# Performance work log

Measured on AMD Instinct MI355X. Metric: run time of the kernel, lower is better.

## Reference

```python
import jax, jax.numpy as jnp
import numpy as np
import math

B, H, S, DIM = 1, 16, 2048, 128

def _clin(xr, xi, wr, wi, br, bi):
    # complex linear: F.linear semantics -> x @ W.T
    out_r = xr @ wr.T - xi @ wi.T + br
    out_i = xr @ wi.T + xi @ wr.T + bi
    return out_r, out_i

def setup_inputs() -> dict:
    key = jax.random.key(0)
    ks = jax.random.split(key, 32)
    shp = (B, H, S, DIM)
    names = ["q_r", "q_i", "k_r", "k_i", "v_r", "v_i", "pe_q_r", "pe_q_i", "pe_k_r", "pe_k_i"]
    d = {n: jax.random.normal(ks[i], shp, jnp.float32) for i, n in enumerate(names)}
    wscale = 1.0 / math.sqrt(DIM)
    i = 10
    for p in ["q", "k", "v", "g", "o"]:
        d[p + "w_r"] = jax.random.normal(ks[i], (DIM, DIM), jnp.float32) * wscale; i += 1
        d[p + "w_i"] = jax.random.normal(ks[i], (DIM, DIM), jnp.float32) * wscale; i += 1
        d[p + "b_r"] = jnp.zeros((DIM,), jnp.float32)
        d[p + "b_i"] = jnp.zeros((DIM,), jnp.float32)
    return d

def reference(q_r, q_i, k_r, k_i, v_r, v_i, pe_q_r, pe_q_i, pe_k_r, pe_k_i,
              qw_r, qw_i, qb_r, qb_i, kw_r, kw_i, kb_r, kb_i,
              vw_r, vw_i, vb_r, vb_i, gw_r, gw_i, gb_r, gb_i,
              ow_r, ow_i, ob_r, ob_i):
    scale = DIM ** -0.5
    qr, qi = _clin(q_r, q_i, qw_r, qw_i, qb_r, qb_i)
    kr, ki = _clin(k_r, k_i, kw_r, kw_i, kb_r, kb_i)
    vr, vi = _clin(v_r, v_i, vw_r, vw_i, vb_r, vb_i)
    qr = qr + pe_q_r; qi = qi + pe_q_i
    kr = kr + pe_k_r; ki = ki + pe_k_i
    # complex QK^H -> real/imag parts, shapes [B,H,S,S]
    sr = jnp.einsum('bhqd,bhkd->bhqk', qr, kr) + jnp.einsum('bhqd,bhkd->bhqk', qi, ki)
    si = jnp.einsum('bhqd,bhkd->bhqk', qi, kr) - jnp.einsum('bhqd,bhkd->bhqk', qr, ki)
    scores = jnp.sqrt(sr * sr + si * si + 1e-8) * scale  # magnitude scores
    attn = jax.nn.softmax(scores, axis=-1)
    ar = attn @ vr
    ai = attn @ vi
    gr, gi = _clin(q_r, q_i, gw_r, gw_i, gb_r, gb_i)  # gate from raw q
    gar = gr * ar - gi * ai
    gai = gr * ai + gi * ar
    out_r, out_i = _clin(gar, gai, ow_r, ow_i, ob_r, ob_i)
    return (out_r, out_i, gr, gi)
```

## Files before the change

kernel.cpp:

```cpp
#include <hip/hip_runtime.h>
#include <math.h>

#define HH 16
#define SS 2048
#define DD 128
#define NROWS (HH * SS)
#define OUTSZ (HH * SS * DD)

typedef __attribute__((ext_vector_type(8))) short bf16x8;
typedef __attribute__((ext_vector_type(4))) float f32x4;
typedef __attribute__((ext_vector_type(8))) unsigned short u16x8;

#define MFMA16(a, b, c) __builtin_amdgcn_mfma_f32_16x16x32_bf16(a, b, c, 0, 0, 0)

__device__ __forceinline__ unsigned short f2bf(float f) {
    unsigned u = __float_as_uint(f);
    return (unsigned short)((u + 0x7FFFu + ((u >> 16) & 1u)) >> 16);
}
__device__ __forceinline__ bf16x8 negf(bf16x8 a) {
    bf16x8 r;
#pragma unroll
    for (int j = 0; j < 8; ++j) r[j] = (short)(a[j] ^ (short)0x8000);
    return r;
}

struct ClinPtrs {
    const float* xr; const float* xi;
    const float* wr; const float* wi;
    const float* br; const float* bi;
    const float* per; const float* pei;
    void* yr; void* yi;
    int outbf;
};

struct RawA { float4 v[16]; };

__device__ __forceinline__ void load_tile(RawA& r, const float* xr, const float* xi,
                                          long rbase, int quad) {
#pragma unroll
    for (int dk = 0; dk < 4; ++dk) {
        const long o = rbase + dk * 32 + quad * 8;
        r.v[dk * 4 + 0] = *(const float4*)(xr + o);
        r.v[dk * 4 + 1] = *(const float4*)(xr + o + 4);
        r.v[dk * 4 + 2] = *(const float4*)(xi + o);
        r.v[dk * 4 + 3] = *(const float4*)(xi + o + 4);
    }
}
__device__ __forceinline__ void conv_tile(const RawA& r, bf16x8* xrf, bf16x8* xif) {
#pragma unroll
    for (int dk = 0; dk < 4; ++dk) {
        const float4 a0 = r.v[dk * 4 + 0], a1 = r.v[dk * 4 + 1];
        const float4 b0 = r.v[dk * 4 + 2], b1 = r.v[dk * 4 + 3];
        const float fr[8] = {a0.x, a0.y, a0.z, a0.w, a1.x, a1.y, a1.z, a1.w};
        const float fi[8] = {b0.x, b0.y, b0.z, b0.w, b1.x, b1.y, b1.z, b1.w};
#pragma unroll
        for (int j = 0; j < 8; ++j) {
            xrf[dk][j] = (short)f2bf(fr[j]);
            xif[dk][j] = (short)f2bf(fi[j]);
        }
    }
}

__global__ __launch_bounds__(512, 2)
void clin_stream(ClinPtrs P0, ClinPtrs P1, ClinPtrs P2, ClinPtrs P3) {
    __shared__ unsigned short wsh[2][DD][136];

    const int py = blockIdx.y;
    const ClinPtrs P = (py == 0) ? P0 : (py == 1) ? P1 : (py == 2) ? P2 : P3;

    const int t = threadIdx.x;
    const int w = t >> 6, lane = t & 63;
    const int lm = lane & 15, quad = lane >> 4;
    const long blockRow0 = (long)blockIdx.x * 512;

    RawA rawA, rawB;
    load_tile(rawA, P.xr, P.xi, (blockRow0 + w * 16 + lm) * DD, quad);

#pragma unroll
    for (int u = 0; u < 8; ++u) {
        const int f = t + 512 * u;
        const int c = f >> 11;
        const int rem = f & 2047;
        const int row = rem >> 4;
        const int g8 = (rem & 15) * 8;
        const float* src = (c ? P.wi : P.wr) + (long)row * DD + g8;
        const float4 a = *(const float4*)src;
        const float4 b = *(const float4*)(src + 4);
        unsigned short tmp[8] = {f2bf(a.x), f2bf(a.y), f2bf(a.z), f2bf(a.w),
                                 f2bf(b.x), f2bf(b.y), f2bf(b.z), f2bf(b.w)};
        *(u16x8*)&wsh[c][row][g8] = *(u16x8*)tmp;
    }
    __syncthreads();

    const f32x4 z = {0.f, 0.f, 0.f, 0.f};

#pragma unroll
    for (int tt = 0; tt < 4; ++tt) {
        RawA& cur = (tt & 1) ? rawB : rawA;
        RawA& nxt = (tt & 1) ? rawA : rawB;
        if (tt < 3)
            load_tile(nxt, P.xr, P.xi,
                      (blockRow0 + (tt + 1) * 128 + w * 16 + lm) * DD, quad);

        bf16x8 xrf[4], xif[4];
        conv_tile(cur, xrf, xif);

        f32x4 Or[8], Oi[8];
#pragma unroll
        for (int nt = 0; nt < 8; ++nt) { Or[nt] = z; Oi[nt] = z; }

#pragma unroll
        for (int dk = 0; dk < 4; ++dk) {
            const bf16x8 nxi = negf(xif[dk]);
            const int off = dk * 32 + quad * 8;
#pragma unroll
            for (int nt = 0; nt < 8; ++nt) {
                const bf16x8 wrf = *(bf16x8*)&wsh[0][nt * 16 + lm][off];
                const bf16x8 wif = *(bf16x8*)&wsh[1][nt * 16 + lm][off];
                Or[nt] = MFMA16(xrf[dk], wrf, Or[nt]);
                Or[nt] = MFMA16(nxi,     wif, Or[nt]);
                Oi[nt] = MFMA16(xrf[dk], wif, Oi[nt]);
                Oi[nt] = MFMA16(xif[dk], wrf, Oi[nt]);
            }
        }

        const long m0 = blockRow0 + tt * 128 + w * 16;
#pragma unroll
        for (int nt = 0; nt < 8; ++nt) {
            const int c = nt * 16 + lm;
            const float bra = P.br[c], bia = P.bi[c];
#pragma unroll
            for (int reg = 0; reg < 4; ++reg) {
                const long R = m0 + quad * 4 + reg;
                float vr = Or[nt][reg] + bra;
                float vi = Oi[nt][reg] + bia;
                if (P.per != nullptr) {
                    vr += P.per[R * DD + c];
                    vi += P.pei[R * DD + c];
                }
                if (P.outbf) {
                    ((unsigned short*)P.yr)[R * DD + c] = f2bf(vr);
                    ((unsigned short*)P.yi)[R * DD + c] = f2bf(vi);
                } else {
                    ((float*)P.yr)[R * DD + c] = vr;
                    ((float*)P.yi)[R * DD + c] = vi;
                }
            }
        }
    }
}

__global__ __launch_bounds__(512, 2)
void clin_gate(const float* __restrict__ xr, const float* __restrict__ xi,
               const float* __restrict__ gr, const float* __restrict__ gi,
               const float* __restrict__ wr, const float* __restrict__ wi,
               const float* __restrict__ br, const float* __restrict__ bi,
               float* __restrict__ yr, float* __restrict__ yi) {
    __shared__ unsigned short wsh[2][DD][136];

    const int t = threadIdx.x;
#pragma unroll
    for (int u = 0; u < 8; ++u) {
        const int f = t + 512 * u;
        const int c = f >> 11;
        const int rem = f & 2047;
        const int row = rem >> 4;
        const int g8 = (rem & 15) * 8;
        const float* src = (c ? wi : wr) + (long)row * DD + g8;
        const float4 a = *(const float4*)src;
        const float4 b = *(const float4*)(src + 4);
        unsigned short tmp[8] = {f2bf(a.x), f2bf(a.y), f2bf(a.z), f2bf(a.w),
                                 f2bf(b.x), f2bf(b.y), f2bf(b.z), f2bf(b.w)};
        *(u16x8*)&wsh[c][row][g8] = *(u16x8*)tmp;
    }

    const int w = t >> 6, lane = t & 63;
    const int lm = lane & 15, quad = lane >> 4;
    const long m0 = (long)blockIdx.x * 128 + w * 16;

    bf16x8 xrf[4], xif[4];
    {
        const long rbase = (m0 + lm) * DD;
#pragma unroll
        for (int dk = 0; dk < 4; ++dk) {
            const long o = rbase + dk * 32 + quad * 8;
            const float4 a0 = *(const float4*)(xr + o);
            const float4 a1 = *(const float4*)(xr + o + 4);
            const float4 b0 = *(const float4*)(xi + o);
            const float4 b1 = *(const float4*)(xi + o + 4);
            const float4 c0v = *(const float4*)(gr + o);
            const float4 c1v = *(const float4*)(gr + o + 4);
            const float4 d0v = *(const float4*)(gi + o);
            const float4 d1v = *(const float4*)(gi + o + 4);
            const float fr[8] = {a0.x, a0.y, a0.z, a0.w, a1.x, a1.y, a1.z, a1.w};
            const float fi[8] = {b0.x, b0.y, b0.z, b0.w, b1.x, b1.y, b1.z, b1.w};
            const float ur[8] = {c0v.x, c0v.y, c0v.z, c0v.w, c1v.x, c1v.y, c1v.z, c1v.w};
            const float ui[8] = {d0v.x, d0v.y, d0v.z, d0v.w, d1v.x, d1v.y, d1v.z, d1v.w};
#pragma unroll
            for (int j = 0; j < 8; ++j) {
                const float pr = fr[j] * ur[j] - fi[j] * ui[j];
                const float pi = fr[j] * ui[j] + fi[j] * ur[j];
                xrf[dk][j] = (short)f2bf(pr);
                xif[dk][j] = (short)f2bf(pi);
            }
        }
    }

    f32x4 Or[8], Oi[8];
    const f32x4 z = {0.f, 0.f, 0.f, 0.f};
#pragma unroll
    for (int nt = 0; nt < 8; ++nt) { Or[nt] = z; Oi[nt] = z; }

    __syncthreads();

#pragma unroll
    for (int dk = 0; dk < 4; ++dk) {
        const bf16x8 nxi = negf(xif[dk]);
        const int off = dk * 32 + quad * 8;
#pragma unroll
        for (int nt = 0; nt < 8; ++nt) {
            const bf16x8 wrf = *(bf16x8*)&wsh[0][nt * 16 + lm][off];
            const bf16x8 wif = *(bf16x8*)&wsh[1][nt * 16 + lm][off];
            Or[nt] = MFMA16(xrf[dk], wrf, Or[nt]);
            Or[nt] = MFMA16(nxi,     wif, Or[nt]);
            Oi[nt] = MFMA16(xrf[dk], wif, Oi[nt]);
            Oi[nt] = MFMA16(xif[dk], wrf, Oi[nt]);
        }
    }

#pragma unroll
    for (int nt = 0; nt < 8; ++nt) {
        const int c = nt * 16 + lm;
        const float bra = br[c], bia = bi[c];
#pragma unroll
        for (int reg = 0; reg < 4; ++reg) {
            const long R = m0 + quad * 4 + reg;
            yr[R * DD + c] = Or[nt][reg] + bra;
            yi[R * DD + c] = Oi[nt][reg] + bia;
        }
    }
}

__global__ __launch_bounds__(512, 2)
void attn_mfma(const unsigned short* __restrict__ qr, const unsigned short* __restrict__ qi,
               const unsigned short* __restrict__ kr, const unsigned short* __restrict__ ki,
               const unsigned short* __restrict__ vr, const unsigned short* __restrict__ vi,
               float* __restrict__ out_r, float* __restrict__ out_i) {
    __shared__ unsigned short ks[2][2][32][136];
    __shared__ unsigned short vt[2][2][DD][40];
    __shared__ unsigned short ps[128][40];

    const int t = threadIdx.x;
    const int w = t >> 6, lane = t & 63;
    const int lm = lane & 15, quad = lane >> 4;

    const int bid = blockIdx.x;
    const int xcd = bid & 7;
    const int rr = bid >> 3;
    const int qt = rr & 15;
    const int h  = xcd + 8 * (rr >> 4);
    const long hbase = (long)h * SS * DD;
    const int q0 = qt * 128;
    const float scale = 0.08838834764831845f;

    int kC[2], kR[2], kG[2];
    const unsigned short* kp[2];
#pragma unroll
    for (int u = 0; u < 2; ++u) {
        const int f = t + 512 * u;
        kC[u] = f >> 9;
        kR[u] = (f & 511) >> 4;
        kG[u] = (f & 15) * 8;
        kp[u] = (kC[u] ? ki : kr) + hbase + (long)kR[u] * DD + kG[u];
    }
    const int vC = t >> 8;
    const int vS2 = (t & 15) * 2;
    const int vD8 = ((t >> 4) & 15) * 8;
    const unsigned short* vp = (vC ? vi : vr) + hbase + (long)vS2 * DD + vD8;

    u16x8 kA0, kA1, vA0, vA1;
    kA0 = *(const u16x8*)(kp[0]);
    kA1 = *(const u16x8*)(kp[1]);
    vA0 = *(const u16x8*)(vp);
    vA1 = *(const u16x8*)(vp + DD);

    bf16x8 qrf[4], qif[4];
    {
        const long rb = hbase + (long)(q0 + w * 16 + lm) * DD;
#pragma unroll
        for (int dk = 0; dk < 4; ++dk) {
            qrf[dk] = *(const bf16x8*)(qr + rb + dk * 32 + quad * 8);
            qif[dk] = *(const bf16x8*)(qi + rb + dk * 32 + quad * 8);
        }
    }

    f32x4 Or[8], Oi[8];
    const f32x4 z = {0.f, 0.f, 0.f, 0.f};
#pragma unroll
    for (int nt = 0; nt < 8; ++nt) { Or[nt] = z; Oi[nt] = z; }
    float l_st[4] = {0.f, 0.f, 0.f, 0.f};

#pragma unroll
    for (int u = 0; u < 2; ++u)
        *(u16x8*)&ks[0][kC[u]][kR[u]][kG[u]] = (u ? kA1 : kA0);
#pragma unroll
    for (int j = 0; j < 8; ++j) {
        const unsigned val = (unsigned)(unsigned short)vA0[j] |
                             ((unsigned)(unsigned short)vA1[j] << 16);
        *(unsigned*)&vt[0][vC][vD8 + j][vS2] = val;
    }
    __syncthreads();

    for (int kt = 0; kt < SS / 32; ++kt) {
        const int b = kt & 1;
        if (kt + 1 < SS / 32) {
            const long koff = (long)(kt + 1) * 32 * DD;
            kA0 = *(const u16x8*)(kp[0] + koff);
            kA1 = *(const u16x8*)(kp[1] + koff);
            vA0 = *(const u16x8*)(vp + koff);
            vA1 = *(const u16x8*)(vp + koff + DD);
        }

        f32x4 sr0 = z, sr1 = z, si0 = z, si1 = z;
#pragma unroll
        for (int dk = 0; dk < 4; ++dk) {
            const int off = dk * 32 + quad * 8;
            const bf16x8 kr0 = *(bf16x8*)&ks[b][0][lm][off];
            const bf16x8 ki0 = *(bf16x8*)&ks[b][1][lm][off];
            const bf16x8 kr1 = *(bf16x8*)&ks[b][0][16 + lm][off];
            const bf16x8 ki1 = *(bf16x8*)&ks[b][1][16 + lm][off];
            const bf16x8 nq = negf(qrf[dk]);
            sr0 = MFMA16(qrf[dk], kr0, sr0);  sr0 = MFMA16(qif[dk], ki0, sr0);
            si0 = MFMA16(qif[dk], kr0, si0);  si0 = MFMA16(nq, ki0, si0);
            sr1 = MFMA16(qrf[dk], kr1, sr1);  sr1 = MFMA16(qif[dk], ki1, sr1);
            si1 = MFMA16(qif[dk], kr1, si1);  si1 = MFMA16(nq, ki1, si1);
        }

#pragma unroll
        for (int reg = 0; reg < 4; ++reg) {
            const float s0 = __builtin_amdgcn_sqrtf(
                fmaf(sr0[reg], sr0[reg], fmaf(si0[reg], si0[reg], 1e-8f))) * scale;
            const float s1 = __builtin_amdgcn_sqrtf(
                fmaf(sr1[reg], sr1[reg], fmaf(si1[reg], si1[reg], 1e-8f))) * scale;
            const float p0 = __expf(s0);
            const float p1 = __expf(s1);
            l_st[reg] += p0 + p1;
            ps[w * 16 + quad * 4 + reg][lm]      = f2bf(p0);
            ps[w * 16 + quad * 4 + reg][16 + lm] = f2bf(p1);
        }

        const bf16x8 pf = *(bf16x8*)&ps[w * 16 + lm][quad * 8];
#pragma unroll
        for (int nt = 0; nt < 8; ++nt) {
            const bf16x8 vrf = *(bf16x8*)&vt[b][0][nt * 16 + lm][quad * 8];
            const bf16x8 vif = *(bf16x8*)&vt[b][1][nt * 16 + lm][quad * 8];
            Or[nt] = MFMA16(pf, vrf, Or[nt]);
            Oi[nt] = MFMA16(pf, vif, Oi[nt]);
        }

        if (kt + 1 < SS / 32) {
            __syncthreads();
#pragma unroll
            for (int u = 0; u < 2; ++u)
                *(u16x8*)&ks[b ^ 1][kC[u]][kR[u]][kG[u]] = (u ? kA1 : kA0);
#pragma unroll
            for (int j = 0; j < 8; ++j) {
                const unsigned val = (unsigned)(unsigned short)vA0[j] |
                                     ((unsigned)(unsigned short)vA1[j] << 16);
                *(unsigned*)&vt[b ^ 1][vC][vD8 + j][vS2] = val;
            }
            __syncthreads();
        }
    }

    float linv[4];
#pragma unroll
    for (int reg = 0; reg < 4; ++reg) {
        float l = l_st[reg];
#pragma unroll
        for (int off = 1; off < 16; off <<= 1) l += __shfl_xor(l, off);
        linv[reg] = 1.f / l;
    }
    const long ob = hbase + (long)(q0 + w * 16) * DD;
#pragma unroll
    for (int nt = 0; nt < 8; ++nt) {
        const int c = nt * 16 + lm;
#pragma unroll
        for (int reg = 0; reg < 4; ++reg) {
            const long R = ob + (long)(quad * 4 + reg) * DD + c;
            out_r[R] = Or[nt][reg] * linv[reg];
            out_i[R] = Oi[nt][reg] * linv[reg];
        }
    }
}

extern "C" void kernel_launch(void* const* d_in, const int* in_sizes, int n_in,
                              void* d_out, int out_size, void* d_ws, size_t ws_size,
                              hipStream_t stream) {
    const float* q_r    = (const float*)d_in[0];
    const float* q_i    = (const float*)d_in[1];
    const float* k_r    = (const float*)d_in[2];
    const float* k_i    = (const float*)d_in[3];
    const float* v_r    = (const float*)d_in[4];
    const float* v_i    = (const float*)d_in[5];
    const float* pe_q_r = (const float*)d_in[6];
    const float* pe_q_i = (const float*)d_in[7];
    const float* pe_k_r = (const float*)d_in[8];
    const float* pe_k_i = (const float*)d_in[9];
    const float* qw_r = (const float*)d_in[10];
    const float* qw_i = (const float*)d_in[11];
    const float* qb_r = (const float*)d_in[12];
    const float* qb_i = (const float*)d_in[13];
    const float* kw_r = (const float*)d_in[14];
    const float* kw_i = (const float*)d_in[15];
    const float* kb_r = (const float*)d_in[16];
    const float* kb_i = (const float*)d_in[17];
    const float* vw_r = (const float*)d_in[18];
    const float* vw_i = (const float*)d_in[19];
    const float* vb_r = (const float*)d_in[20];
    const float* vb_i = (const float*)d_in[21];
    const float* gw_r = (const float*)d_in[22];
    const float* gw_i = (const float*)d_in[23];
    const float* gb_r = (const float*)d_in[24];
    const float* gb_i = (const float*)d_in[25];
    const float* ow_r = (const float*)d_in[26];
    const float* ow_i = (const float*)d_in[27];
    const float* ob_r = (const float*)d_in[28];
    const float* ob_i = (const float*)d_in[29];

    float* out_r = (float*)d_out;
    float* out_i = out_r + (long)OUTSZ;
    float* g_r   = out_r + 2L * OUTSZ;
    float* g_i   = out_r + 3L * OUTSZ;

    unsigned short* ws = (unsigned short*)d_ws;
    unsigned short* pqr = ws + 0L * OUTSZ;
    unsigned short* pqi = ws + 1L * OUTSZ;
    unsigned short* pkr = ws + 2L * OUTSZ;
    unsigned short* pki = ws + 3L * OUTSZ;
    unsigned short* pvr = ws + 4L * OUTSZ;
    unsigned short* pvi = ws + 5L * OUTSZ;

    const dim3 blk(512);

    ClinPtrs P0 = {q_r, q_i, qw_r, qw_i, qb_r, qb_i, pe_q_r, pe_q_i, pqr, pqi, 1};
    ClinPtrs P1 = {k_r, k_i, kw_r, kw_i, kb_r, kb_i, pe_k_r, pe_k_i, pkr, pki, 1};
    ClinPtrs P2 = {v_r, v_i, vw_r, vw_i, vb_r, vb_i, nullptr, nullptr, pvr, pvi, 1};
    ClinPtrs P3 = {q_r, q_i, gw_r, gw_i, gb_r, gb_i, nullptr, nullptr, g_r, g_i, 0};

    clin_stream<<<dim3(64, 4), blk, 0, stream>>>(P0, P1, P2, P3);

    attn_mfma<<<dim3((SS / 128) * HH), blk, 0, stream>>>(
        pqr, pqi, pkr, pki, pvr, pvi, out_r, out_i);

    clin_gate<<<dim3(NROWS / 128), blk, 0, stream>>>(
        g_r, g_i, out_r, out_i, ow_r, ow_i, ob_r, ob_i, out_r, out_i);
}
```

Measured before the change: 457.7 us.

## Fuse gating into attention epilogue and simplify projection kernel to one tile

The complex gate multiply moves into the attention epilogue, which now reads the fp32 gate and writes the gated result as bf16 to workspace. The output projection then loads bf16 directly instead of reading four fp32 tensors and multiplying. This cuts fp32 round trips through global memory. The projection kernel also drops its 4-tile software-pipelined loop in favour of one tile per block with a larger grid, trading prefetch overlap for more blocks and more weight reloads.

```diff
diff --git a/kernel.cpp b/kernel.cpp
--- a/kernel.cpp
+++ b/kernel.cpp
@@ -33,49 +33,14 @@
     int outbf;
 };
 
-struct RawA { float4 v[16]; };
-
-__device__ __forceinline__ void load_tile(RawA& r, const float* xr, const float* xi,
-                                          long rbase, int quad) {
-#pragma unroll
-    for (int dk = 0; dk < 4; ++dk) {
-        const long o = rbase + dk * 32 + quad * 8;
-        r.v[dk * 4 + 0] = *(const float4*)(xr + o);
-        r.v[dk * 4 + 1] = *(const float4*)(xr + o + 4);
-        r.v[dk * 4 + 2] = *(const float4*)(xi + o);
-        r.v[dk * 4 + 3] = *(const float4*)(xi + o + 4);
-    }
-}
-__device__ __forceinline__ void conv_tile(const RawA& r, bf16x8* xrf, bf16x8* xif) {
-#pragma unroll
-    for (int dk = 0; dk < 4; ++dk) {
-        const float4 a0 = r.v[dk * 4 + 0], a1 = r.v[dk * 4 + 1];
-        const float4 b0 = r.v[dk * 4 + 2], b1 = r.v[dk * 4 + 3];
-        const float fr[8] = {a0.x, a0.y, a0.z, a0.w, a1.x, a1.y, a1.z, a1.w};
-        const float fi[8] = {b0.x, b0.y, b0.z, b0.w, b1.x, b1.y, b1.z, b1.w};
-#pragma unroll
-        for (int j = 0; j < 8; ++j) {
-            xrf[dk][j] = (short)f2bf(fr[j]);
-            xif[dk][j] = (short)f2bf(fi[j]);
-        }
-    }
-}
-
 __global__ __launch_bounds__(512, 2)
-void clin_stream(ClinPtrs P0, ClinPtrs P1, ClinPtrs P2, ClinPtrs P3) {
+void clin_proj(ClinPtrs P0, ClinPtrs P1, ClinPtrs P2, ClinPtrs P3) {
     __shared__ unsigned short wsh[2][DD][136];
 
     const int py = blockIdx.y;
     const ClinPtrs P = (py == 0) ? P0 : (py == 1) ? P1 : (py == 2) ? P2 : P3;
 
     const int t = threadIdx.x;
-    const int w = t >> 6, lane = t & 63;
-    const int lm = lane & 15, quad = lane >> 4;
-    const long blockRow0 = (long)blockIdx.x * 512;
-
-    RawA rawA, rawB;
-    load_tile(rawA, P.xr, P.xi, (blockRow0 + w * 16 + lm) * DD, quad);
-
 #pragma unroll
     for (int u = 0; u < 8; ++u) {
         const int f = t + 512 * u;
@@ -90,72 +55,82 @@
                                  f2bf(b.x), f2bf(b.y), f2bf(b.z), f2bf(b.w)};
         *(u16x8*)&wsh[c][row][g8] = *(u16x8*)tmp;
     }
+
+    const int w = t >> 6, lane = t & 63;
+    const int lm = lane & 15, quad = lane >> 4;
+    const long m0 = (long)blockIdx.x * 128 + w * 16;
+
+    bf16x8 xrf[4], xif[4];
+    {
+        const long rbase = (m0 + lm) * DD;
+#pragma unroll
+        for (int dk = 0; dk < 4; ++dk) {
+            const long o = rbase + dk * 32 + quad * 8;
+            const float4 a0 = *(const float4*)(P.xr + o);
+            const float4 a1 = *(const float4*)(P.xr + o + 4);
+            const float4 b0 = *(const float4*)(P.xi + o);
+            const float4 b1 = *(const float4*)(P.xi + o + 4);
+            const float fr[8] = {a0.x, a0.y, a0.z, a0.w, a1.x, a1.y, a1.z, a1.w};
+            const float fi[8] = {b0.x, b0.y, b0.z, b0.w, b1.x, b1.y, b1.z, b1.w};
+#pragma unroll
+            for (int j = 0; j < 8; ++j) {
+                xrf[dk][j] = (short)f2bf(fr[j]);
+                xif[dk][j] = (short)f2bf(fi[j]);
+            }
+        }
+    }
+
+    f32x4 Or[8], Oi[8];
+    const f32x4 z = {0.f, 0.f, 0.f, 0.f};
+#pragma unroll
+    for (int nt = 0; nt < 8; ++nt) { Or[nt] = z; Oi[nt] = z; }
+
     __syncthreads();
 
-    const f32x4 z = {0.f, 0.f, 0.f, 0.f};
-
-#pragma unroll
-    for (int tt = 0; tt < 4; ++tt) {
-        RawA& cur = (tt & 1) ? rawB : rawA;
-        RawA& nxt = (tt & 1) ? rawA : rawB;
-        if (tt < 3)
-            load_tile(nxt, P.xr, P.xi,
-                      (blockRow0 + (tt + 1) * 128 + w * 16 + lm) * DD, quad);
-
-        bf16x8 xrf[4], xif[4];
-        conv_tile(cur, xrf, xif);
-
-        f32x4 Or[8], Oi[8];
-#pragma unroll
-        for (int nt = 0; nt < 8; ++nt) { Or[nt] = z; Oi[nt] = z; }
-
-#pragma unroll
-        for (int dk = 0; dk < 4; ++dk) {
-            const bf16x8 nxi = negf(xif[dk]);
-            const int off = dk * 32 + quad * 8;
-#pragma unroll
-            for (int nt = 0; nt < 8; ++nt) {
-                const bf16x8 wrf = *(bf16x8*)&wsh[0][nt * 16 + lm][off];
-                const bf16x8 wif = *(bf16x8*)&wsh[1][nt * 16 + lm][off];
-                Or[nt] = MFMA16(xrf[dk], wrf, Or[nt]);
-                Or[nt] = MFMA16(nxi,     wif, Or[nt]);
-                Oi[nt] = MFMA16(xrf[dk], wif, Oi[nt]);
-                Oi[nt] = MFMA16(xif[dk], wrf, Oi[nt]);
+#pragma unroll
+    for (int dk = 0; dk < 4; ++dk) {
+        const bf16x8 nxi = negf(xif[dk]);
+        const int off = dk * 32 + quad * 8;
+#pragma unroll
+        for (int nt = 0; nt < 8; ++nt) {
+            const bf16x8 wrf = *(bf16x8*)&wsh[0][nt * 16 + lm][off];
+            const bf16x8 wif = *(bf16x8*)&wsh[1][nt * 16 + lm][off];
+            Or[nt] = MFMA16(xrf[dk], wrf, Or[nt]);
+            Or[nt] = MFMA16(nxi,     wif, Or[nt]);
+            Oi[nt] = MFMA16(xrf[dk], wif, Oi[nt]);
+            Oi[nt] = MFMA16(xif[dk], wrf, Oi[nt]);
+        }
+    }
+
+#pragma unroll
+    for (int nt = 0; nt < 8; ++nt) {
+        const int c = nt * 16 + lm;
+        const float bra = P.br[c], bia = P.bi[c];
+#pragma unroll
+        for (int reg = 0; reg < 4; ++reg) {
+            const long R = m0 + quad * 4 + reg;
+            float vr = Or[nt][reg] + bra;
+            float vi = Oi[nt][reg] + bia;
+            if (P.per != nullptr) {
+                vr += P.per[R * DD + c];
+                vi += P.pei[R * DD + c];
             }
-        }
-
-        const long m0 = blockRow0 + tt * 128 + w * 16;
-#pragma unroll
-        for (int nt = 0; nt < 8; ++nt) {
-            const int c = nt * 16 + lm;
-            const float bra = P.br[c], bia = P.bi[c];
-#pragma unroll
-            for (int reg = 0; reg < 4; ++reg) {
-                const long R = m0 + quad * 4 + reg;
-                float vr = Or[nt][reg] + bra;
-                float vi = Oi[nt][reg] + bia;
-                if (P.per != nullptr) {
-                    vr += P.per[R * DD + c];
-                    vi += P.pei[R * DD + c];
-                }
-                if (P.outbf) {
-                    ((unsigned short*)P.yr)[R * DD + c] = f2bf(vr);
-                    ((unsigned short*)P.yi)[R * DD + c] = f2bf(vi);
-                } else {
-                    ((float*)P.yr)[R * DD + c] = vr;
-                    ((float*)P.yi)[R * DD + c] = vi;
-                }
+            if (P.outbf) {
+                ((unsigned short*)P.yr)[R * DD + c] = f2bf(vr);
+                ((unsigned short*)P.yi)[R * DD + c] = f2bf(vi);
+            } else {
+                ((float*)P.yr)[R * DD + c] = vr;
+                ((float*)P.yi)[R * DD + c] = vi;
             }
         }
     }
 }
 
 __global__ __launch_bounds__(512, 2)
-void clin_gate(const float* __restrict__ xr, const float* __restrict__ xi,
-               const float* __restrict__ gr, const float* __restrict__ gi,
-               const float* __restrict__ wr, const float* __restrict__ wi,
-               const float* __restrict__ br, const float* __restrict__ bi,
-               float* __restrict__ yr, float* __restrict__ yi) {
+void clin_obf(const unsigned short* __restrict__ xr, const unsigned short* __restrict__ xi,
+              const float* __restrict__ wr, const float* __restrict__ wi,
+              const float* __restrict__ br, const float* __restrict__ bi,
+              float* __restrict__ yr, float* __restrict__ yi) {
     __shared__ unsigned short wsh[2][DD][136];
 
     const int t = threadIdx.x;
@@ -180,29 +155,11 @@
 
     bf16x8 xrf[4], xif[4];
     {
-        const long rbase = (m0 + lm) * DD;
+        const long rbase = (m0 + lm) * DD + quad * 8;
 #pragma unroll
         for (int dk = 0; dk < 4; ++dk) {
-            const long o = rbase + dk * 32 + quad * 8;
-            const float4 a0 = *(const float4*)(xr + o);
-            const float4 a1 = *(const float4*)(xr + o + 4);
-            const float4 b0 = *(const float4*)(xi + o);
-            const float4 b1 = *(const float4*)(xi + o + 4);
-            const float4 c0v = *(const float4*)(gr + o);
-            const float4 c1v = *(const float4*)(gr + o + 4);
-            const float4 d0v = *(const float4*)(gi + o);
-            const float4 d1v = *(const float4*)(gi + o + 4);
-            const float fr[8] = {a0.x, a0.y, a0.z, a0.w, a1.x, a1.y, a1.z, a1.w};
-            const float fi[8] = {b0.x, b0.y, b0.z, b0.w, b1.x, b1.y, b1.z, b1.w};
-            const float ur[8] = {c0v.x, c0v.y, c0v.z, c0v.w, c1v.x, c1v.y, c1v.z, c1v.w};
-            const float ui[8] = {d0v.x, d0v.y, d0v.z, d0v.w, d1v.x, d1v.y, d1v.z, d1v.w};
-#pragma unroll
-            for (int j = 0; j < 8; ++j) {
-                const float pr = fr[j] * ur[j] - fi[j] * ui[j];
-                const float pi = fr[j] * ui[j] + fi[j] * ur[j];
-                xrf[dk][j] = (short)f2bf(pr);
-                xif[dk][j] = (short)f2bf(pi);
-            }
+            xrf[dk] = *(const bf16x8*)(xr + rbase + dk * 32);
+            xif[dk] = *(const bf16x8*)(xi + rbase + dk * 32);
         }
     }
 
@@ -245,7 +202,8 @@
 void attn_mfma(const unsigned short* __restrict__ qr, const unsigned short* __restrict__ qi,
                const unsigned short* __restrict__ kr, const unsigned short* __restrict__ ki,
                const unsigned short* __restrict__ vr, const unsigned short* __restrict__ vi,
-               float* __restrict__ out_r, float* __restrict__ out_i) {
+               const float* __restrict__ g_r, const float* __restrict__ g_i,
+               unsigned short* __restrict__ gar, unsigned short* __restrict__ gai) {
     __shared__ unsigned short ks[2][2][32][136];
     __shared__ unsigned short vt[2][2][DD][40];
     __shared__ unsigned short ps[128][40];
@@ -388,8 +346,12 @@
 #pragma unroll
         for (int reg = 0; reg < 4; ++reg) {
             const long R = ob + (long)(quad * 4 + reg) * DD + c;
-            out_r[R] = Or[nt][reg] * linv[reg];
-            out_i[R] = Oi[nt][reg] * linv[reg];
+            const float ar = Or[nt][reg] * linv[reg];
+            const float ai = Oi[nt][reg] * linv[reg];
+            const float g1 = g_r[R];
+            const float g2 = g_i[R];
+            gar[R] = f2bf(g1 * ar - g2 * ai);
+            gai[R] = f2bf(g1 * ai + g2 * ar);
         }
     }
 }
@@ -440,6 +402,8 @@
     unsigned short* pki = ws + 3L * OUTSZ;
     unsigned short* pvr = ws + 4L * OUTSZ;
     unsigned short* pvi = ws + 5L * OUTSZ;
+    unsigned short* gar = ws + 6L * OUTSZ;
+    unsigned short* gai = ws + 7L * OUTSZ;
 
     const dim3 blk(512);
 
@@ -448,11 +412,11 @@
     ClinPtrs P2 = {v_r, v_i, vw_r, vw_i, vb_r, vb_i, nullptr, nullptr, pvr, pvi, 1};
     ClinPtrs P3 = {q_r, q_i, gw_r, gw_i, gb_r, gb_i, nullptr, nullptr, g_r, g_i, 0};
 
-    clin_stream<<<dim3(64, 4), blk, 0, stream>>>(P0, P1, P2, P3);
+    clin_proj<<<dim3(NROWS / 128, 4), blk, 0, stream>>>(P0, P1, P2, P3);
 
     attn_mfma<<<dim3((SS / 128) * HH), blk, 0, stream>>>(
-        pqr, pqi, pkr, pki, pvr, pvi, out_r, out_i);
-
-    clin_gate<<<dim3(NROWS / 128), blk, 0, stream>>>(
-        g_r, g_i, out_r, out_i, ow_r, ow_i, ob_r, ob_i, out_r, out_i);
-}
+        pqr, pqi, pkr, pki, pvr, pvi, g_r, g_i, gar, gai);
+
+    clin_obf<<<dim3(NROWS / 128), blk, 0, stream>>>(
+        gar, gai, ow_r, ow_i, ob_r, ob_i, out_r, out_i);
+}
```

Result: faster. 419.6 us (-8.3%).
